# Kernel tuning notes

Hardware: AMD Instinct MI355X
Metric: run time of the kernel (lower is better)

## Reference

```python
import jax, jax.numpy as jnp
import numpy as np

B, WAYS, SHOTS, C, H, W = 64, 10, 5, 128, 32, 32


def setup_inputs() -> dict:
    key = jax.random.key(0)
    k1, k2, k3 = jax.random.split(key, 3)
    q = jax.random.normal(k1, (B, C, H, W), dtype=jnp.float32)
    support = jax.random.normal(k2, (WAYS, SHOTS, C, H, W), dtype=jnp.float32)
    conv_w = jax.random.normal(k3, (H * W,), dtype=jnp.float32) * 0.03
    return {"q": q, "support": support, "conv_w": conv_w}


def reference(q, support, conv_w):
    b, c, h, w = q.shape
    ways, shots = support.shape[:2]
    hw = h * w
    # --- cal_covariance: per-class channel covariance ---
    # [ways, shots, C, h, w] -> [ways, C, shots*h*w]
    s = support.transpose(0, 2, 1, 3, 4).reshape(ways, c, shots * hw)
    s = s - s.mean(axis=2, keepdims=True)
    denom = jnp.float32(shots * hw - 1)
    cov = jnp.einsum('jcn,jdn->jcd', s, s) / denom  # [ways, C, C]
    # --- cal_similarity: per-pixel quadratic form diag(Q^T Sigma Q) ---
    qf = q.reshape(b, c, hw)
    qn = qf / jnp.linalg.norm(qf, axis=2, keepdims=True)  # L2 norm per channel row
    t = jnp.einsum('jcd,bdp->bjcp', cov, qn)              # [B, ways, C, hw]
    sim = jnp.einsum('bcp,bjcp->bjp', qn, t)              # diagonal only: [B, ways, hw]
    # --- classifier1: LeakyReLU(0.2) -> Dropout (eval identity) -> Conv1d(1,1,k=hw,stride=hw,bias=False) ---
    x = sim.reshape(b, ways * hw)
    x = jnp.where(x >= 0, x, 0.2 * x)
    out = jnp.einsum('bjp,p->bj', x.reshape(b, ways, hw), conv_w)  # [B, ways]
    return out
```

## Files before the change

### kernel.cpp

```cpp
#include <hip/hip_runtime.h>

typedef unsigned short u16;
typedef unsigned int u32;
typedef __attribute__((ext_vector_type(8))) short bf16x8;
typedef __attribute__((ext_vector_type(4))) short bf16x4v;
typedef __attribute__((ext_vector_type(4))) float f32x4;

#define NWAYS 10
#define NC 128
#define NHW 1024

__device__ __forceinline__ u16 f2bf(float f) {
  u32 u = __builtin_bit_cast(u32, f);
  return (u16)((u + 0x7fffu + ((u >> 16) & 1u)) >> 16);
}
__device__ __forceinline__ float bf2f(u16 h) {
  u32 u = ((u32)h) << 16;
  return __builtin_bit_cast(float, u);
}

__global__ __launch_bounds__(512) void k_phase1(const float* __restrict__ sup,
                                                const float* __restrict__ q,
                                                const float* __restrict__ cw,
                                                u16* __restrict__ Gpartb,
                                                float* __restrict__ mpart,
                                                u16* __restrict__ Wrawb,
                                                float* __restrict__ ss,
                                                float* __restrict__ out) {
  __shared__ u16 smem[NC * 256];
  __shared__ float saux[NC];
  int bid = blockIdx.x;
  int t = threadIdx.x;
  int w = t >> 6, l = t & 63, lr = l & 15, lg = l >> 4;

  if (bid < 100) {
    int j = bid / 10, chunk = bid % 10;
    int shot = chunk >> 1, p0 = (chunk & 1) * 512;
    const float* srcbase = sup + ((size_t)(j * 5 + shot) * NC) * NHW + p0;
    if (t < NC) saux[t] = 0.f;
    __syncthreads();

    f32x4 acc[8];
#pragma unroll
    for (int bt = 0; bt < 8; ++bt) acc[bt] = (f32x4){0.f, 0.f, 0.f, 0.f};

#pragma unroll 1
    for (int sub = 0; sub < 2; ++sub) {
      const float* srcsub = srcbase + sub * 256;
#pragma unroll 4
      for (int it = 0; it < 16; ++it) {
        int c = it * 8 + w;
        float4 v = *(const float4*)(srcsub + (size_t)c * NHW + l * 4);
        int nl = l * 4;
        int idx = c * 256 + (((nl >> 3) ^ (c & 15)) << 3) + (nl & 7);
        bf16x4v h;
        h[0] = (short)f2bf(v.x); h[1] = (short)f2bf(v.y);
        h[2] = (short)f2bf(v.z); h[3] = (short)f2bf(v.w);
        *(bf16x4v*)&smem[idx] = h;
        float s = v.x + v.y + v.z + v.w;
#pragma unroll
        for (int m = 1; m <= 32; m <<= 1) s += __shfl_xor(s, m, 64);
        if (l == 0) saux[c] += s;
      }
      __syncthreads();
#pragma unroll
      for (int kb = 0; kb < 8; ++kb) {
        int nn = kb * 32 + lg * 8;
        int arow = w * 16 + lr;
        bf16x8 fa = *(const bf16x8*)&smem[arow * 256 + (((nn >> 3) ^ (arow & 15)) << 3)];
        bf16x8 fb[8];
#pragma unroll
        for (int bt = 0; bt < 8; ++bt) {
          int drow = bt * 16 + lr;
          fb[bt] = *(const bf16x8*)&smem[drow * 256 + (((nn >> 3) ^ (drow & 15)) << 3)];
        }
#pragma unroll
        for (int bt = 0; bt < 8; ++bt)
          acc[bt] = __builtin_amdgcn_mfma_f32_16x16x32_bf16(fa, fb[bt], acc[bt], 0, 0, 0);
      }
      __syncthreads();
    }
    if (t < NC) mpart[(size_t)bid * NC + t] = saux[t];
    u16* gp = Gpartb + ((size_t)bid << 14);
#pragma unroll
    for (int bt = 0; bt < 8; ++bt)
#pragma unroll
      for (int r = 0; r < 4; ++r) {
        int cr = w * 16 + lg * 4 + r;
        int d = bt * 16 + lr;
        gp[cr * NC + d] = f2bf(acc[bt][r]);
      }
  } else {
    int bid2 = bid - 100;
    if (bid2 < 2) {
      int o = bid2 * 512 + t;
      if (o < 64 * NWAYS) out[o] = 0.f;
    }
    int b = bid2 >> 1, half = bid2 & 1;
    u16* traw = smem;
    u16* twgt = smem + 16384;
    const float* base = q + (size_t)b * NC * NHW + half * 512;
    const float* cwb = cw + half * 512;

    float4 v[8];
    auto load_chunk = [&](int chunk) {
#pragma unroll
      for (int it = 0; it < 8; ++it) {
        int idx = it * 512 + t;
        int c = idx >> 5, pos = idx & 31;
        v[it] = *(const float4*)(base + (size_t)c * NHW + chunk * 128 + pos * 4);
      }
    };
    auto store_chunk = [&](int chunk) {
#pragma unroll
      for (int it = 0; it < 8; ++it) {
        int idx = it * 512 + t;
        int c = idx >> 5, pos = idx & 31;
        float4 vv = v[it];
        float4 wv = *(const float4*)(cwb + chunk * 128 + pos * 4);
        int nl = pos * 4;
        int off = c * 128 + (((nl >> 3) ^ (c & 15)) << 3) + (nl & 7);
        bf16x4v hr, hw;
        hr[0] = (short)f2bf(vv.x); hr[1] = (short)f2bf(vv.y);
        hr[2] = (short)f2bf(vv.z); hr[3] = (short)f2bf(vv.w);
        hw[0] = (short)f2bf(vv.x * wv.x); hw[1] = (short)f2bf(vv.y * wv.y);
        hw[2] = (short)f2bf(vv.z * wv.z); hw[3] = (short)f2bf(vv.w * wv.w);
        *(bf16x4v*)&traw[off] = hr;
        *(bf16x4v*)&twgt[off] = hw;
        float s = vv.x * vv.x + vv.y * vv.y + vv.z * vv.z + vv.w * vv.w;
#pragma unroll
        for (int m = 1; m <= 16; m <<= 1) s += __shfl_xor(s, m, 64);
        if ((l & 31) == 0) saux[c] += s;
      }
    };

    load_chunk(0);
    if (t < NC) saux[t] = 0.f;
    __syncthreads();
    store_chunk(0);
    __syncthreads();

    f32x4 acc[8];
#pragma unroll
    for (int bt = 0; bt < 8; ++bt) acc[bt] = (f32x4){0.f, 0.f, 0.f, 0.f};
#pragma unroll 1
    for (int chunk = 0; chunk < 4; ++chunk) {
      if (chunk < 3) load_chunk(chunk + 1);
#pragma unroll
      for (int kb = 0; kb < 4; ++kb) {
        int nn = kb * 32 + lg * 8;
        int arow = w * 16 + lr;
        bf16x8 fa = *(const bf16x8*)&twgt[arow * 128 + (((nn >> 3) ^ (arow & 15)) << 3)];
        bf16x8 fb[8];
#pragma unroll
        for (int bt = 0; bt < 8; ++bt) {
          int drow = bt * 16 + lr;
          fb[bt] = *(const bf16x8*)&traw[drow * 128 + (((nn >> 3) ^ (drow & 15)) << 3)];
        }
#pragma unroll
        for (int bt = 0; bt < 8; ++bt)
          acc[bt] = __builtin_amdgcn_mfma_f32_16x16x32_bf16(fa, fb[bt], acc[bt], 0, 0, 0);
      }
      __syncthreads();
      if (chunk < 3) { store_chunk(chunk + 1); __syncthreads(); }
    }

    if (t < NC) ss[(size_t)(half * 64 + b) * NC + t] = saux[t];
    u16* wb = Wrawb + ((size_t)(half * 64 + b) << 14);
#pragma unroll
    for (int bt = 0; bt < 8; ++bt)
#pragma unroll
      for (int r = 0; r < 4; ++r) {
        int cr = w * 16 + lg * 4 + r;
        int d = bt * 16 + lr;
        wb[cr * NC + d] = f2bf(acc[bt][r]);
      }
  }
}

__global__ __launch_bounds__(256) void k_fin(const u16* __restrict__ Gpartb,
                                             const float* __restrict__ mpart,
                                             u16* __restrict__ covb) {
  __shared__ float msd[NC];
  int j = blockIdx.x >> 4, rg = blockIdx.x & 15;
  int t = threadIdx.x;
  if (t < NC) {
    float s = 0.f;
#pragma unroll
    for (int k = 0; k < 10; ++k) s += mpart[(size_t)(j * 10 + k) * NC + t];
    msd[t] = s;
  }
  __syncthreads();
  int e = rg * 1024 + t * 4;
  int c = e >> 7, d0 = e & 127;
  float g[4] = {0.f, 0.f, 0.f, 0.f};
#pragma unroll
  for (int k = 0; k < 10; ++k) {
    bf16x4v v = *(const bf16x4v*)(Gpartb + (((size_t)(j * 10 + k)) << 14) + e);
#pragma unroll
    for (int r = 0; r < 4; ++r) g[r] += bf2f((u16)v[r]);
  }
  bf16x4v o;
#pragma unroll
  for (int r = 0; r < 4; ++r)
    o[r] = (short)f2bf((g[r] - msd[c] * msd[d0 + r] * (1.0f / 5120.0f)) * (1.0f / 5119.0f));
  *(bf16x4v*)(covb + (((size_t)j) << 14) + e) = o;
}

__global__ __launch_bounds__(256) void k_wndot(const u16* __restrict__ Wrawb,
                                               const float* __restrict__ ss,
                                               const u16* __restrict__ covb,
                                               float* __restrict__ out) {
  __shared__ float rnl[NC];
  __shared__ float red[4 * NWAYS];
  int b = blockIdx.x >> 2, rg = blockIdx.x & 3;
  int t = threadIdx.x;
  int w = t >> 6, l = t & 63;
  if (t < NC) {
    float s = ss[(size_t)b * NC + t] + ss[(size_t)(64 + b) * NC + t];
    rnl[t] = rsqrtf(s);
  }
  __syncthreads();
  int e = rg * 4096 + t * 16;
  int c = e >> 7, d0 = e & 127;
  float wn[16];
#pragma unroll
  for (int k = 0; k < 16; ++k) wn[k] = 0.f;
#pragma unroll
  for (int qr = 0; qr < 2; ++qr) {
    const u16* src = Wrawb + (((size_t)(qr * 64 + b)) << 14) + e;
    bf16x8 v0 = *(const bf16x8*)src;
    bf16x8 v1 = *(const bf16x8*)(src + 8);
#pragma unroll
    for (int k = 0; k < 8; ++k) { wn[k] += bf2f((u16)v0[k]); wn[8 + k] += bf2f((u16)v1[k]); }
  }
  float rc = rnl[c];
#pragma unroll
  for (int k = 0; k < 16; ++k) wn[k] *= rc * rnl[d0 + k];

  float acc[NWAYS];
#pragma unroll
  for (int j = 0; j < NWAYS; ++j) {
    const u16* cj = covb + ((size_t)j << 14) + e;
    bf16x8 c0 = *(const bf16x8*)cj;
    bf16x8 c1 = *(const bf16x8*)(cj + 8);
    float s = 0.f;
#pragma unroll
    for (int k = 0; k < 8; ++k) s += wn[k] * bf2f((u16)c0[k]) + wn[8 + k] * bf2f((u16)c1[k]);
    acc[j] = s;
  }
#pragma unroll
  for (int j = 0; j < NWAYS; ++j)
#pragma unroll
    for (int m = 1; m <= 32; m <<= 1) acc[j] += __shfl_xor(acc[j], m, 64);
  if (l == 0)
#pragma unroll
    for (int j = 0; j < NWAYS; ++j) red[w * NWAYS + j] = acc[j];
  __syncthreads();
  if (t < NWAYS)
    atomicAdd(&out[b * NWAYS + t],
              red[t] + red[NWAYS + t] + red[2 * NWAYS + t] + red[3 * NWAYS + t]);
}

extern "C" void kernel_launch(void* const* d_in, const int* in_sizes, int n_in,
                              void* d_out, int out_size, void* d_ws, size_t ws_size,
                              hipStream_t stream) {
  (void)in_sizes; (void)n_in; (void)out_size; (void)ws_size;
  const float* q = (const float*)d_in[0];
  const float* sup = (const float*)d_in[1];
  const float* cw = (const float*)d_in[2];
  float* out = (float*)d_out;

  char* p = (char*)d_ws;
  u16* Gpartb = (u16*)p;    p += (size_t)100 * 16384 * 2;
  float* mpart = (float*)p; p += (size_t)100 * 128 * 4;
  u16* covb = (u16*)p;      p += (size_t)10 * 16384 * 2;
  u16* Wrawb = (u16*)p;     p += (size_t)128 * 16384 * 2;
  float* ssb = (float*)p;

  k_phase1<<<228, 512, 0, stream>>>(sup, q, cw, Gpartb, mpart, Wrawb, ssb, out);
  k_fin<<<160, 256, 0, stream>>>(Gpartb, mpart, covb);
  k_wndot<<<256, 256, 0, stream>>>(Wrawb, ssb, covb, out);
}
```

Baseline: 36.06 us.

## Software-pipeline support covariance loads into registers across 128-column chunks

Restructures the phase-1 covariance blocks to process support data in four 128-column chunks, issuing global loads for the next chunk into registers while MFMA runs on the current chunk in LDS. This aims to hide global memory latency behind the bf16 matrix multiplies instead of serializing load, convert and compute. It costs more registers (eight float4 per thread held across the MFMA loop) and extra barriers per chunk.

```diff
diff --git a/kernel.cpp b/kernel.cpp
--- a/kernel.cpp
+++ b/kernel.cpp
@@ -34,52 +34,71 @@
   int w = t >> 6, l = t & 63, lr = l & 15, lg = l >> 4;
 
   if (bid < 100) {
-    int j = bid / 10, chunk = bid % 10;
-    int shot = chunk >> 1, p0 = (chunk & 1) * 512;
-    const float* srcbase = sup + ((size_t)(j * 5 + shot) * NC) * NHW + p0;
+    int j = bid / 10, cid = bid % 10;
+    int shot = cid >> 1, p0 = (cid & 1) * 512;
+    const float* base = sup + ((size_t)(j * 5 + shot) * NC) * NHW + p0;
+    u16* traw = smem;
+
+    float4 v[8];
+    auto load_chunk = [&](int chunk) {
+#pragma unroll
+      for (int it = 0; it < 8; ++it) {
+        int idx = it * 512 + t;
+        int c = idx >> 5, pos = idx & 31;
+        v[it] = *(const float4*)(base + (size_t)c * NHW + chunk * 128 + pos * 4);
+      }
+    };
+    auto store_chunk = [&](int chunk) {
+      (void)chunk;
+#pragma unroll
+      for (int it = 0; it < 8; ++it) {
+        int idx = it * 512 + t;
+        int c = idx >> 5, pos = idx & 31;
+        float4 vv = v[it];
+        int nl = pos * 4;
+        int off = c * 128 + (((nl >> 3) ^ (c & 15)) << 3) + (nl & 7);
+        bf16x4v hr;
+        hr[0] = (short)f2bf(vv.x); hr[1] = (short)f2bf(vv.y);
+        hr[2] = (short)f2bf(vv.z); hr[3] = (short)f2bf(vv.w);
+        *(bf16x4v*)&traw[off] = hr;
+        float s = vv.x + vv.y + vv.z + vv.w;
+#pragma unroll
+        for (int m = 1; m <= 16; m <<= 1) s += __shfl_xor(s, m, 64);
+        if ((l & 31) == 0) saux[c] += s;
+      }
+    };
+
+    load_chunk(0);
     if (t < NC) saux[t] = 0.f;
     __syncthreads();
+    store_chunk(0);
+    __syncthreads();
 
     f32x4 acc[8];
 #pragma unroll
     for (int bt = 0; bt < 8; ++bt) acc[bt] = (f32x4){0.f, 0.f, 0.f, 0.f};
-
 #pragma unroll 1
-    for (int sub = 0; sub < 2; ++sub) {
-      const float* srcsub = srcbase + sub * 256;
-#pragma unroll 4
-      for (int it = 0; it < 16; ++it) {
-        int c = it * 8 + w;
-        float4 v = *(const float4*)(srcsub + (size_t)c * NHW + l * 4);
-        int nl = l * 4;
-        int idx = c * 256 + (((nl >> 3) ^ (c & 15)) << 3) + (nl & 7);
-        bf16x4v h;
-        h[0] = (short)f2bf(v.x); h[1] = (short)f2bf(v.y);
-        h[2] = (short)f2bf(v.z); h[3] = (short)f2bf(v.w);
-        *(bf16x4v*)&smem[idx] = h;
-        float s = v.x + v.y + v.z + v.w;
-#pragma unroll
-        for (int m = 1; m <= 32; m <<= 1) s += __shfl_xor(s, m, 64);
-        if (l == 0) saux[c] += s;
-      }
-      __syncthreads();
-#pragma unroll
-      for (int kb = 0; kb < 8; ++kb) {
+    for (int chunk = 0; chunk < 4; ++chunk) {
+      if (chunk < 3) load_chunk(chunk + 1);
+#pragma unroll
+      for (int kb = 0; kb < 4; ++kb) {
         int nn = kb * 32 + lg * 8;
         int arow = w * 16 + lr;
-        bf16x8 fa = *(const bf16x8*)&smem[arow * 256 + (((nn >> 3) ^ (arow & 15)) << 3)];
+        bf16x8 fa = *(const bf16x8*)&traw[arow * 128 + (((nn >> 3) ^ (arow & 15)) << 3)];
         bf16x8 fb[8];
 #pragma unroll
         for (int bt = 0; bt < 8; ++bt) {
           int drow = bt * 16 + lr;
-          fb[bt] = *(const bf16x8*)&smem[drow * 256 + (((nn >> 3) ^ (drow & 15)) << 3)];
+          fb[bt] = *(const bf16x8*)&traw[drow * 128 + (((nn >> 3) ^ (drow & 15)) << 3)];
         }
 #pragma unroll
         for (int bt = 0; bt < 8; ++bt)
           acc[bt] = __builtin_amdgcn_mfma_f32_16x16x32_bf16(fa, fb[bt], acc[bt], 0, 0, 0);
       }
       __syncthreads();
+      if (chunk < 3) { store_chunk(chunk + 1); __syncthreads(); }
     }
+
     if (t < NC) mpart[(size_t)bid * NC + t] = saux[t];
     u16* gp = Gpartb + ((size_t)bid << 14);
 #pragma unroll
```

Measured after the change: 30.02 us (median of 2 runs). -16.7%, faster.
